# Performance work log

Hardware: AMD Instinct MI355X
Metric: run time of the kernel (lower is better)

## Reference

```python
import jax, jax.numpy as jnp
import numpy as np

G = 64        # voxel grid resolution per axis
Z_DIM = 32    # latent (feature) dim per voxel
HID = 128     # decoder hidden dim
NUM_BLOCKS = 5
NQ = 500000   # number of query points

# 8 trilinear corner offsets (matches the 3D branch of differentiable_interpolation)
_OFFSETS = np.array([[0,0,0],[0,0,1],[0,1,0],[0,1,1],[1,0,0],[1,0,1],[1,1,0],[1,1,1]], dtype=np.float32)


def setup_inputs() -> dict:
    key = jax.random.key(0)
    ks = jax.random.split(key, 14)
    s = 0.02
    z_feats = jax.random.normal(ks[0], (G * G * G, Z_DIM), dtype=jnp.float32)
    # queries in [0, G-1) so that floor+1 <= G-1 (all 8 corners in-grid)
    query = jax.random.uniform(ks[1], (NQ, 3), dtype=jnp.float32) * (G - 1 - 1e-3)
    fc_p_w = jax.random.normal(ks[2], (HID, Z_DIM), dtype=jnp.float32) * s
    fc_p_b = jax.random.normal(ks[3], (HID,), dtype=jnp.float32) * s
    fc_c_w = jax.random.normal(ks[4], (NUM_BLOCKS, HID, Z_DIM), dtype=jnp.float32) * s
    fc_c_b = jax.random.normal(ks[5], (NUM_BLOCKS, HID), dtype=jnp.float32) * s
    fc0_w = jax.random.normal(ks[6], (NUM_BLOCKS, HID, HID), dtype=jnp.float32) * s
    fc0_b = jax.random.normal(ks[7], (NUM_BLOCKS, HID), dtype=jnp.float32) * s
    fc1_w = jax.random.normal(ks[8], (NUM_BLOCKS, HID, HID), dtype=jnp.float32) * s
    fc1_b = jax.random.normal(ks[9], (NUM_BLOCKS, HID), dtype=jnp.float32) * s
    fc_out_w = jax.random.normal(ks[10], (1, HID), dtype=jnp.float32) * s
    fc_out_b = jax.random.normal(ks[11], (1,), dtype=jnp.float32) * s
    return {"z_feats": z_feats, "query": query,
            "fc_p_w": fc_p_w, "fc_p_b": fc_p_b,
            "fc_c_w": fc_c_w, "fc_c_b": fc_c_b,
            "fc0_w": fc0_w, "fc0_b": fc0_b,
            "fc1_w": fc1_w, "fc1_b": fc1_b,
            "fc_out_w": fc_out_w, "fc_out_b": fc_out_b,
            "grid_size": G}


def _interpolate(z_feats, query, grid_size):
    # trilinear gather-interpolate over a fully occupied voxel grid
    qf = jnp.floor(query)
    rel = query - qf                                  # [Nq,3]
    base = qf.astype(jnp.int32)                       # [Nq,3]
    off = jnp.asarray(_OFFSETS)                       # [8,3]
    corner = base[:, None, :] + off[None].astype(jnp.int32)  # [Nq,8,3]
    # weight per corner: prod_d ((1-o) + (2o-1)*rel) = prod_d (o ? rel : 1-rel)
    w = jnp.prod(jnp.where(off[None] > 0.5, rel[:, None, :], 1.0 - rel[:, None, :]), axis=-1)  # [Nq,8]
    flat = (corner[..., 0] * grid_size + corner[..., 1]) * grid_size + corner[..., 2]          # [Nq,8]
    feats = z_feats[flat]                             # [Nq,8,Z] irregular gather
    return jnp.einsum('nk,nkd->nd', w, feats)         # [Nq,Z]


def _decode(latent, fc_p_w, fc_p_b, fc_c_w, fc_c_b, fc0_w, fc0_b, fc1_w, fc1_b, fc_out_w, fc_out_b):
    net = latent @ fc_p_w.T + fc_p_b
    for i in range(fc_c_w.shape[0]):
        net = net + latent @ fc_c_w[i].T + fc_c_b[i]
        # ResnetBlockFC: x + fc_1(relu(fc_0(relu(x))))  (size_in==size_out => identity shortcut)
        h = jax.nn.relu(net) @ fc0_w[i].T + fc0_b[i]
        dx = jax.nn.relu(h) @ fc1_w[i].T + fc1_b[i]
        net = net + dx
    out = jax.nn.leaky_relu(net, 0.2) @ fc_out_w.T + fc_out_b  # leaky_activation=True
    return out[:, 0]


def reference(z_feats, query, fc_p_w, fc_p_b, fc_c_w, fc_c_b, fc0_w, fc0_b, fc1_w, fc1_b, fc_out_w, fc_out_b, grid_size):
    latent = _interpolate(z_feats, query, grid_size)
    return _decode(latent, fc_p_w, fc_p_b, fc_c_w, fc_c_b, fc0_w, fc0_b, fc1_w, fc1_b, fc_out_w, fc_out_b)
```

## Files before the change

kernel.cpp:

```cpp
#include <hip/hip_runtime.h>


#define TQ 256
#define BLOCK 512
#define HD 128
#define ZD 32
#define NBLK 5
#define GR 64

typedef _Float16 f16x8 __attribute__((ext_vector_type(8)));
typedef _Float16 f16x4 __attribute__((ext_vector_type(4)));
typedef float f32x4 __attribute__((ext_vector_type(4)));

#define OFF_P 0
#define OFF_C 4096
#define OFF_0 24576
#define OFF_1 106496
#define WS_HALVES 188416

__global__ void convert_weights(const float* __restrict__ fc_p_w,
                                const float* __restrict__ fc_c_w,
                                const float* __restrict__ fc0_w,
                                const float* __restrict__ fc1_w,
                                _Float16* __restrict__ ws) {
  int i = blockIdx.x * 256 + threadIdx.x;
  if (i >= WS_HALVES) return;
  if (i < 4096) {
    ws[OFF_P + i] = (_Float16)fc_p_w[i];
    return;
  }
  i -= 4096;
  if (i < 20480) {
    ws[OFF_C + i] = (_Float16)fc_c_w[i];
    return;
  }
  i -= 20480;
  if (i < 81920) {
    const int row = i >> 7;
    const int col = i & 127;
    const int gs = col >> 3, e = col & 7;
    ws[OFF_0 + i] = (_Float16)fc0_w[(row << 7) + (((gs ^ (row & 7)) << 3) | e)];
    return;
  }
  i -= 81920;
  {
    const int c4 = i >> 13;
    const int li = c4 >> 1, h = c4 & 1;
    const int r = (i & 8191) >> 6;
    const int cc = i & 63;
    const int gs = cc >> 3, e = cc & 7;
    const int k = (h << 6) + (((gs ^ (r & 7)) << 3) | e);
    ws[OFF_1 + i] = (_Float16)fc1_w[li * 16384 + (r << 7) + k];
  }
}

struct SMem {
  _Float16 NET[TQ * HD];
  _Float16 H[TQ * 64];
  _Float16 WB[3][8192];
};

__device__ __forceinline__ void stage_chunk(char* lds, const char* g, int t) {
  __builtin_amdgcn_global_load_lds(
      (const __attribute__((address_space(1))) void*)(g + t * 16),
      (__attribute__((address_space(3))) void*)(lds + t * 16), 16, 0, 0);
  __builtin_amdgcn_global_load_lds(
      (const __attribute__((address_space(1))) void*)(g + 8192 + t * 16),
      (__attribute__((address_space(3))) void*)(lds + 8192 + t * 16), 16, 0, 0);
}

__device__ __forceinline__ f16x4 relu_pack(const f32x4& a) {
  f16x4 r;
#pragma unroll
  for (int i = 0; i < 4; ++i) r[i] = (_Float16)fmaxf(a[i], 0.f);
  return r;
}

__device__ __forceinline__ void fc0_half(SMem& sm, int slot,
                                         const float* __restrict__ b0p, int qe,
                                         int lr, int lg) {
  f32x4 hacc[4][2];
#pragma unroll
  for (int jt = 0; jt < 4; ++jt) {
    const f32x4 bv = *(const f32x4*)(b0p + 16 * jt + 4 * lg);
    hacc[jt][0] = bv;
    hacc[jt][1] = bv;
  }
#pragma unroll
  for (int ks = 0; ks < 4; ++ks) {
    f16x8 af[4];
#pragma unroll
    for (int jt = 0; jt < 4; ++jt)
      af[jt] = *(const f16x8*)((const char*)sm.WB[slot] + (16 * jt + lr) * 256 +
                               (((4 * ks + lg) ^ (lr & 7)) << 4));
    f16x8 xf[2];
#pragma unroll
    for (int q2 = 0; q2 < 2; ++q2) {
      const int q = qe + 16 * q2 + lr;
      xf[q2] = *(const f16x8*)((const char*)sm.NET + q * 256 +
                               (((4 * ks + lg) ^ (q & 7)) << 4));
    }
#pragma unroll
    for (int jt = 0; jt < 4; ++jt)
#pragma unroll
      for (int q2 = 0; q2 < 2; ++q2)
        hacc[jt][q2] = __builtin_amdgcn_mfma_f32_16x16x32_f16(af[jt], xf[q2],
                                                              hacc[jt][q2], 0, 0, 0);
  }
#pragma unroll
  for (int jt = 0; jt < 4; ++jt)
#pragma unroll
    for (int q2 = 0; q2 < 2; ++q2) {
      const int q = qe + 16 * q2 + lr;
      const int G = (2 * jt + (lg >> 1)) ^ (q & 7);
      *(f16x4*)((char*)sm.H + q * 128 + (G << 4) + ((lg & 1) << 3)) =
          relu_pack(hacc[jt][q2]);
    }
}

__device__ __forceinline__ void fc1_half(SMem& sm, int slot, f32x4 (&acc)[4][4],
                                         int j0, int q0, int lr, int lg) {
#pragma unroll
  for (int ks = 0; ks < 2; ++ks) {
    f16x8 a1[4];
#pragma unroll
    for (int jt = 0; jt < 4; ++jt)
      a1[jt] = *(const f16x8*)((const char*)sm.WB[slot] + (j0 + 16 * jt + lr) * 128 +
                               (((4 * ks + lg) ^ (lr & 7)) << 4));
    f16x8 hf[4];
#pragma unroll
    for (int qt = 0; qt < 4; ++qt) {
      const int q = q0 + 16 * qt + lr;
      hf[qt] = *(const f16x8*)((const char*)sm.H + q * 128 +
                               (((4 * ks + lg) ^ (q & 7)) << 4));
    }
#pragma unroll
    for (int jt = 0; jt < 4; ++jt)
#pragma unroll
      for (int qt = 0; qt < 4; ++qt)
        acc[jt][qt] = __builtin_amdgcn_mfma_f32_16x16x32_f16(a1[jt], hf[qt],
                                                             acc[jt][qt], 0, 0, 0);
  }
}

__global__ __launch_bounds__(BLOCK, 2) void patch_decoder_kernel(
    const float* __restrict__ z_feats, const float* __restrict__ query,
    const _Float16* __restrict__ ws, const float* __restrict__ fc_p_b,
    const float* __restrict__ fc_c_b, const float* __restrict__ fc0_b,
    const float* __restrict__ fc1_b, const float* __restrict__ fc_out_w,
    const float* __restrict__ fc_out_b, float* __restrict__ out, int nq) {
  __shared__ SMem sm;
  const int t = threadIdx.x;
  const int w = t >> 6;
  const int l = t & 63;
  const int lr = l & 15, lg = l >> 4;
  const int j0 = (w & 1) << 6;
  const int q0 = (w >> 1) << 6;
  const int qe = w << 5;
  const int qbase = blockIdx.x * TQ;

  const char* w0base = (const char*)(ws + OFF_0);
  const char* w1base = (const char*)(ws + OFF_1);

  stage_chunk((char*)sm.WB[0], w0base, t);
  stage_chunk((char*)sm.WB[1], w1base, t);
  stage_chunk((char*)sm.WB[2], w0base + 16384, t);

  {
    const int q = t >> 1, s = t & 1;
    const int qg = qbase + q;
    float acc[16];
#pragma unroll
    for (int e = 0; e < 16; ++e) acc[e] = 0.f;
    if (qg < nq) {
      const float qx = query[qg * 3 + 0];
      const float qy = query[qg * 3 + 1];
      const float qz = query[qg * 3 + 2];
      const float fx = floorf(qx), fy = floorf(qy), fz = floorf(qz);
      const float rx = qx - fx, ry = qy - fy, rz = qz - fz;
      const int bx = (int)fx, by = (int)fy, bz = (int)fz;
      const float wx[2] = {1.f - rx, rx}, wy[2] = {1.f - ry, ry},
                  wz[2] = {1.f - rz, rz};
#pragma unroll
      for (int c = 0; c < 8; ++c) {
        const int ox = (c >> 2) & 1, oy = (c >> 1) & 1, oz = c & 1;
        const float wgt = wx[ox] * wy[oy] * wz[oz];
        const float* f = z_feats +
                         (size_t)(((bx + ox) * GR + (by + oy)) * GR + (bz + oz)) * ZD +
                         s * 16;
#pragma unroll
        for (int v4 = 0; v4 < 4; ++v4) {
          const float4 v = *(const float4*)(f + v4 * 4);
          acc[v4 * 4 + 0] = fmaf(wgt, v.x, acc[v4 * 4 + 0]);
          acc[v4 * 4 + 1] = fmaf(wgt, v.y, acc[v4 * 4 + 1]);
          acc[v4 * 4 + 2] = fmaf(wgt, v.z, acc[v4 * 4 + 2]);
          acc[v4 * 4 + 3] = fmaf(wgt, v.w, acc[v4 * 4 + 3]);
        }
      }
    }
    f16x8 h0, h1;
#pragma unroll
    for (int e = 0; e < 8; ++e) {
      h0[e] = (_Float16)acc[e];
      h1[e] = (_Float16)acc[8 + e];
    }
    char* lb = (char*)sm.H + q * 80 + s * 32;
    *(f16x8*)lb = h0;
    *(f16x8*)(lb + 16) = h1;
  }
  __syncthreads();

  f16x8 latf[4];
#pragma unroll
  for (int qt = 0; qt < 4; ++qt)
    latf[qt] = *(const f16x8*)((const char*)sm.H + (q0 + 16 * qt + lr) * 80 + lg * 16);

  f32x4 acc[4][4];
#pragma unroll
  for (int jt = 0; jt < 4; ++jt) {
    const f32x4 bv = *(const f32x4*)(fc_p_b + j0 + 16 * jt + 4 * lg);
#pragma unroll
    for (int qt = 0; qt < 4; ++qt) acc[jt][qt] = bv;
  }
#pragma unroll
  for (int jt = 0; jt < 4; ++jt) {
    const f16x8 wf = *(const f16x8*)(ws + OFF_P + (j0 + 16 * jt + lr) * 32 + lg * 8);
#pragma unroll
    for (int qt = 0; qt < 4; ++qt)
      acc[jt][qt] = __builtin_amdgcn_mfma_f32_16x16x32_f16(wf, latf[qt], acc[jt][qt],
                                                           0, 0, 0);
  }

#pragma unroll 1
  for (int i = 0; i < NBLK; ++i) {
    const int as = i & 1, bs = as ^ 1;
#pragma unroll
    for (int jt = 0; jt < 4; ++jt) {
      const f16x8 wf =
          *(const f16x8*)(ws + OFF_C + i * 4096 + (j0 + 16 * jt + lr) * 32 + lg * 8);
#pragma unroll
      for (int qt = 0; qt < 4; ++qt)
        acc[jt][qt] = __builtin_amdgcn_mfma_f32_16x16x32_f16(wf, latf[qt],
                                                             acc[jt][qt], 0, 0, 0);
      const f32x4 bv = *(const f32x4*)(fc_c_b + i * HD + j0 + 16 * jt + 4 * lg);
#pragma unroll
      for (int qt = 0; qt < 4; ++qt) acc[jt][qt] += bv;
    }
#pragma unroll
    for (int jt = 0; jt < 4; ++jt)
#pragma unroll
      for (int qt = 0; qt < 4; ++qt) {
        const int q = q0 + 16 * qt + lr;
        const int G = ((j0 >> 3) + 2 * jt + (lg >> 1)) ^ (q & 7);
        *(f16x4*)((char*)sm.NET + q * 256 + (G << 4) + ((lg & 1) << 3)) =
            relu_pack(acc[jt][qt]);
      }
    __syncthreads();

    if (i > 0) stage_chunk((char*)sm.WB[bs], w1base + i * 32768, t);
    fc0_half(sm, as, fc0_b + i * HD, qe, lr, lg);
    __syncthreads();

    stage_chunk((char*)sm.WB[as], w1base + i * 32768 + 16384, t);
    fc1_half(sm, bs, acc, j0, q0, lr, lg);
    __syncthreads();

    if (i + 1 < NBLK)
      stage_chunk((char*)sm.WB[bs], w0base + (i + 1) * 32768, t);
    fc0_half(sm, 2, fc0_b + i * HD + 64, qe, lr, lg);
    __syncthreads();

    if (i + 1 < NBLK)
      stage_chunk((char*)sm.WB[2], w0base + (i + 1) * 32768 + 16384, t);
    fc1_half(sm, as, acc, j0, q0, lr, lg);
#pragma unroll
    for (int jt = 0; jt < 4; ++jt) {
      const f32x4 bv = *(const f32x4*)(fc1_b + i * HD + j0 + 16 * jt + 4 * lg);
#pragma unroll
      for (int qt = 0; qt < 4; ++qt) acc[jt][qt] += bv;
    }
  }

  float* red = (float*)sm.NET;
  {
    float p[4];
#pragma unroll
    for (int qt = 0; qt < 4; ++qt) p[qt] = 0.f;
#pragma unroll
    for (int jt = 0; jt < 4; ++jt) {
      const f32x4 wv = *(const f32x4*)(fc_out_w + j0 + 16 * jt + 4 * lg);
#pragma unroll
      for (int qt = 0; qt < 4; ++qt) {
        const f32x4 a = acc[jt][qt];
#pragma unroll
        for (int r = 0; r < 4; ++r) {
          const float v = (a[r] > 0.f) ? a[r] : 0.2f * a[r];
          p[qt] = fmaf(v, wv[r], p[qt]);
        }
      }
    }
#pragma unroll
    for (int qt = 0; qt < 4; ++qt) {
      p[qt] += __shfl_xor(p[qt], 16);
      p[qt] += __shfl_xor(p[qt], 32);
    }
    __syncthreads();
    if (lg == 0) {
#pragma unroll
      for (int qt = 0; qt < 4; ++qt) red[(w & 1) * 256 + q0 + 16 * qt + lr] = p[qt];
    }
  }
  __syncthreads();
  if (t < TQ) {
    const int qg = qbase + t;
    if (qg < nq) out[qg] = red[t] + red[256 + t] + fc_out_b[0];
  }
}

extern "C" void kernel_launch(void* const* d_in, const int* in_sizes, int n_in,
                              void* d_out, int out_size, void* d_ws,
                              size_t ws_size, hipStream_t stream) {
  const float* z_feats = (const float*)d_in[0];
  const float* query = (const float*)d_in[1];
  const float* fc_p_w = (const float*)d_in[2];
  const float* fc_p_b = (const float*)d_in[3];
  const float* fc_c_w = (const float*)d_in[4];
  const float* fc_c_b = (const float*)d_in[5];
  const float* fc0_w = (const float*)d_in[6];
  const float* fc0_b = (const float*)d_in[7];
  const float* fc1_w = (const float*)d_in[8];
  const float* fc1_b = (const float*)d_in[9];
  const float* fc_out_w = (const float*)d_in[10];
  const float* fc_out_b = (const float*)d_in[11];
  float* out = (float*)d_out;
  _Float16* ws = (_Float16*)d_ws;

  const int nq = in_sizes[1] / 3;

  convert_weights<<<(WS_HALVES + 255) / 256, 256, 0, stream>>>(fc_p_w, fc_c_w,
                                                               fc0_w, fc1_w, ws);
  const int grid = (nq + TQ - 1) / TQ;
  patch_decoder_kernel<<<grid, BLOCK, 0, stream>>>(z_feats, query, ws, fc_p_b,
                                                   fc_c_b, fc0_b, fc1_b, fc_out_w,
                                                   fc_out_b, out, nq);
}
```

Measured before the change: 330.4 us.

## Halve query tile per block and shrink LDS weight buffers to two slots

Halves the block to 128 queries and 256 threads and drops the third weight staging buffer, so each block uses less LDS and more blocks can be resident per CU. The interpolated latents are staged in the NET region instead of H, and the weight chunk schedule is rewritten for two fixed buffers with each stage_chunk issuing four 4 KB loads. The two-buffer schedule gives less prefetch lookahead, and each block now re-stages the full weight set for half as many queries, which doubles total weight traffic.

```diff
diff --git a/kernel.cpp b/kernel.cpp
--- a/kernel.cpp
+++ b/kernel.cpp
@@ -1,8 +1,8 @@
 #include <hip/hip_runtime.h>
 
 
-#define TQ 256
-#define BLOCK 512
+#define TQ 128
+#define BLOCK 256
 #define HD 128
 #define ZD 32
 #define NBLK 5
@@ -57,16 +57,17 @@
 struct SMem {
   _Float16 NET[TQ * HD];
   _Float16 H[TQ * 64];
-  _Float16 WB[3][8192];
+  _Float16 WB[2][8192];
 };
 
 __device__ __forceinline__ void stage_chunk(char* lds, const char* g, int t) {
-  __builtin_amdgcn_global_load_lds(
-      (const __attribute__((address_space(1))) void*)(g + t * 16),
-      (__attribute__((address_space(3))) void*)(lds + t * 16), 16, 0, 0);
-  __builtin_amdgcn_global_load_lds(
-      (const __attribute__((address_space(1))) void*)(g + 8192 + t * 16),
-      (__attribute__((address_space(3))) void*)(lds + 8192 + t * 16), 16, 0, 0);
+#pragma unroll
+  for (int r = 0; r < 4; ++r) {
+    __builtin_amdgcn_global_load_lds(
+        (const __attribute__((address_space(1))) void*)(g + r * 4096 + t * 16),
+        (__attribute__((address_space(3))) void*)(lds + r * 4096 + t * 16), 16,
+        0, 0);
+  }
 }
 
 __device__ __forceinline__ f16x4 relu_pack(const f32x4& a) {
@@ -164,7 +165,6 @@
 
   stage_chunk((char*)sm.WB[0], w0base, t);
   stage_chunk((char*)sm.WB[1], w1base, t);
-  stage_chunk((char*)sm.WB[2], w0base + 16384, t);
 
   {
     const int q = t >> 1, s = t & 1;
@@ -204,7 +204,7 @@
       h0[e] = (_Float16)acc[e];
       h1[e] = (_Float16)acc[8 + e];
     }
-    char* lb = (char*)sm.H + q * 80 + s * 32;
+    char* lb = (char*)sm.NET + q * 80 + s * 32;
     *(f16x8*)lb = h0;
     *(f16x8*)(lb + 16) = h1;
   }
@@ -213,7 +213,8 @@
   f16x8 latf[4];
 #pragma unroll
   for (int qt = 0; qt < 4; ++qt)
-    latf[qt] = *(const f16x8*)((const char*)sm.H + (q0 + 16 * qt + lr) * 80 + lg * 16);
+    latf[qt] =
+        *(const f16x8*)((const char*)sm.NET + (q0 + 16 * qt + lr) * 80 + lg * 16);
 
   f32x4 acc[4][4];
 #pragma unroll
@@ -233,7 +234,6 @@
 
 #pragma unroll 1
   for (int i = 0; i < NBLK; ++i) {
-    const int as = i & 1, bs = as ^ 1;
 #pragma unroll
     for (int jt = 0; jt < 4; ++jt) {
       const f16x8 wf =
@@ -257,22 +257,21 @@
       }
     __syncthreads();
 
-    if (i > 0) stage_chunk((char*)sm.WB[bs], w1base + i * 32768, t);
-    fc0_half(sm, as, fc0_b + i * HD, qe, lr, lg);
+    if (i > 0) stage_chunk((char*)sm.WB[1], w1base + i * 32768, t);
+    fc0_half(sm, 0, fc0_b + i * HD, qe, lr, lg);
     __syncthreads();
 
-    stage_chunk((char*)sm.WB[as], w1base + i * 32768 + 16384, t);
-    fc1_half(sm, bs, acc, j0, q0, lr, lg);
+    stage_chunk((char*)sm.WB[0], w0base + i * 32768 + 16384, t);
+    fc1_half(sm, 1, acc, j0, q0, lr, lg);
     __syncthreads();
 
+    stage_chunk((char*)sm.WB[1], w1base + i * 32768 + 16384, t);
+    fc0_half(sm, 2 - 2, fc0_b + i * HD + 64, qe, lr, lg);
+    __syncthreads();
+
     if (i + 1 < NBLK)
-      stage_chunk((char*)sm.WB[bs], w0base + (i + 1) * 32768, t);
-    fc0_half(sm, 2, fc0_b + i * HD + 64, qe, lr, lg);
-    __syncthreads();
-
-    if (i + 1 < NBLK)
-      stage_chunk((char*)sm.WB[2], w0base + (i + 1) * 32768 + 16384, t);
-    fc1_half(sm, as, acc, j0, q0, lr, lg);
+      stage_chunk((char*)sm.WB[0], w0base + (i + 1) * 32768, t);
+    fc1_half(sm, 1, acc, j0, q0, lr, lg);
 #pragma unroll
     for (int jt = 0; jt < 4; ++jt) {
       const f32x4 bv = *(const f32x4*)(fc1_b + i * HD + j0 + 16 * jt + 4 * lg);
@@ -280,8 +279,9 @@
       for (int qt = 0; qt < 4; ++qt) acc[jt][qt] += bv;
     }
   }
-
-  float* red = (float*)sm.NET;
+  __syncthreads();
+
+  float* red = (float*)sm.H;
   {
     float p[4];
 #pragma unroll
@@ -304,16 +304,16 @@
       p[qt] += __shfl_xor(p[qt], 16);
       p[qt] += __shfl_xor(p[qt], 32);
     }
-    __syncthreads();
     if (lg == 0) {
 #pragma unroll
-      for (int qt = 0; qt < 4; ++qt) red[(w & 1) * 256 + q0 + 16 * qt + lr] = p[qt];
+      for (int qt = 0; qt < 4; ++qt)
+        red[(w & 1) * TQ + q0 + 16 * qt + lr] = p[qt];
     }
   }
   __syncthreads();
   if (t < TQ) {
     const int qg = qbase + t;
-    if (qg < nq) out[qg] = red[t] + red[256 + t] + fc_out_b[0];
+    if (qg < nq) out[qg] = red[t] + red[TQ + t] + fc_out_b[0];
   }
 }
 
```

Measured after the change: 277.7 us. 16.0% less time.
